# Kernel tuning notes

Measured on AMD Instinct MI355X. Metric: run time of the kernel, lower is better.

The kernel has to match this reference:

```python
import jax, jax.numpy as jnp
import numpy as np

N = 100000   # total nodes
E = 1600000  # edges
F_IN = 128   # num_features
HL1 = 128    # hidden
G = 100      # num graphs
GF = 16      # num_global_feats
GH = 32      # global_hl1 (hardcoded in module)


def _gcn_conv(x, W, b, src, dst, n):
    # PyG GCNConv: add self-loops, symmetric deg^{-1/2} normalization,
    # linear transform then normalized scatter-add aggregation, plus bias.
    h = x @ W  # [n, out]
    ones = jnp.ones(src.shape[0], x.dtype)
    deg = jax.ops.segment_sum(ones, dst, num_segments=n) + 1.0  # +1 for self-loop
    dinv = jnp.where(deg > 0, 1.0 / jnp.sqrt(deg), 0.0)
    norm = dinv[src] * dinv[dst]                      # [E]
    agg = jax.ops.segment_sum(h[src] * norm[:, None], dst, num_segments=n)
    agg = agg + h * (dinv * dinv)[:, None]            # self-loop messages (i->i)
    return agg + b


def setup_inputs() -> dict:
    key = jax.random.key(0)
    ks = jax.random.split(key, 24)
    inp = {}
    inp["x"] = jax.random.normal(ks[0], (N, F_IN), jnp.float32)
    inp["edge_index"] = jax.random.randint(ks[1], (2, E), 0, N, jnp.int64)
    inp["batch"] = jnp.sort(jax.random.randint(ks[2], (N,), 0, G, jnp.int32))
    inp["global_feats"] = jax.random.normal(ks[3], (G * GF,), jnp.float32)
    inp["num_graphs"] = G
    s = 0.05
    inp["conv1_W"] = jax.random.normal(ks[4], (F_IN, HL1), jnp.float32) * s
    inp["conv1_b"] = jnp.zeros((HL1,), jnp.float32)
    inp["conv2_W"] = jax.random.normal(ks[5], (HL1, HL1), jnp.float32) * s
    inp["conv2_b"] = jnp.zeros((HL1,), jnp.float32)
    inp["conv3_W"] = jax.random.normal(ks[6], (HL1, HL1), jnp.float32) * s
    inp["conv3_b"] = jnp.zeros((HL1,), jnp.float32)
    inp["conv4_W"] = jax.random.normal(ks[7], (HL1, HL1), jnp.float32) * s
    inp["conv4_b"] = jnp.zeros((HL1,), jnp.float32)
    inp["global1_W"] = jax.random.normal(ks[8], (GF, GH), jnp.float32) * s
    inp["global1_b"] = jnp.zeros((GH,), jnp.float32)
    inp["lin1_W"] = jax.random.normal(ks[9], (HL1, HL1), jnp.float32) * s
    inp["lin1_b"] = jnp.zeros((HL1,), jnp.float32)
    inp["lin2_W"] = jax.random.normal(ks[10], (HL1 + GH, HL1), jnp.float32) * s
    inp["lin2_b"] = jnp.zeros((HL1,), jnp.float32)
    inp["lin3_W"] = jax.random.normal(ks[11], (HL1, HL1), jnp.float32) * s
    inp["lin3_b"] = jnp.zeros((HL1,), jnp.float32)
    inp["lin4_W"] = jax.random.normal(ks[12], (HL1, 1), jnp.float32) * s
    inp["lin4_b"] = jnp.zeros((1,), jnp.float32)
    return inp


def reference(x, edge_index, batch, global_feats, num_graphs,
              conv1_W, conv1_b, conv2_W, conv2_b, conv3_W, conv3_b,
              conv4_W, conv4_b, global1_W, global1_b,
              lin1_W, lin1_b, lin2_W, lin2_b, lin3_W, lin3_b, lin4_W, lin4_b):
    src, dst = edge_index[0], edge_index[1]
    n = x.shape[0]
    relu = jax.nn.relu
    h = relu(_gcn_conv(x, conv1_W, conv1_b, src, dst, n))
    h = relu(_gcn_conv(h, conv2_W, conv2_b, src, dst, n))
    h = relu(_gcn_conv(h, conv3_W, conv3_b, src, dst, n))
    h = relu(_gcn_conv(h, conv4_W, conv4_b, src, dst, n))
    # per-graph sum pooling (vectorized segment-sum instead of python loop)
    pooled = jax.ops.segment_sum(h, batch, num_segments=num_graphs)  # [G, HL1]
    gfs = global_feats.reshape(num_graphs, -1)                        # [G, GF]
    g = relu(gfs @ global1_W + global1_b)                             # [G, GH]
    y = relu(pooled @ lin1_W + lin1_b)
    y = jnp.concatenate([y, g], axis=1)
    y = relu(y @ lin2_W + lin2_b)
    y = relu(y @ lin3_W + lin3_b)
    y = y @ lin4_W + lin4_b
    return y.squeeze(1)  # final_act == 'none'
```

## Files before the change

### kernel.cpp

```cpp
#include <hip/hip_runtime.h>
#include <hip/hip_bf16.h>

#define NN 100000
#define NE 1600000
#define FD 128
#define NG 100
#define GFD 16
#define GHD 32

#define NB 391
#define BCAP 5120

typedef __attribute__((ext_vector_type(8))) _Float16 f16x8;
typedef __attribute__((ext_vector_type(2))) _Float16 f16x2;
typedef __attribute__((ext_vector_type(4))) float f32x4;

static inline int cdiv(int a, int b) { return (a + b - 1) / b; }


__global__ void k_zero_int(int* __restrict__ p, int n) {
  int i = blockIdx.x * blockDim.x + threadIdx.x;
  if (i < n) p[i] = 0;
}

__global__ void k_zero_row(_Float16* __restrict__ Hs) {
  int t = threadIdx.x;
  if (t < FD) Hs[(size_t)NN * FD + t] = (_Float16)0.f;
}

__global__ __launch_bounds__(256) void k_binA(const int* __restrict__ src,
                                              const int* __restrict__ dst,
                                              int* __restrict__ gcur,
                                              unsigned int* __restrict__ stag) {
  __shared__ int cnt[NB];
  __shared__ int gbase[NB];
  __shared__ int cursor[NB];
  int t = threadIdx.x;
  for (int i = t; i < NB; i += 256) cnt[i] = 0;
  __syncthreads();
  int e0 = blockIdx.x * 2048;
  int s[8], d[8], b[8];
#pragma unroll
  for (int j = 0; j < 8; j++) {
    int e = e0 + j * 256 + t;
    if (e < NE) {
      s[j] = src[e];
      d[j] = dst[e];
      b[j] = d[j] >> 8;
      atomicAdd(&cnt[b[j]], 1);
    } else {
      b[j] = -1;
    }
  }
  __syncthreads();
  for (int i = t; i < NB; i += 256) {
    int c = cnt[i];
    gbase[i] = (c > 0) ? atomicAdd(&gcur[i], c) : 0;
    cursor[i] = 0;
  }
  __syncthreads();
#pragma unroll
  for (int j = 0; j < 8; j++) {
    if (b[j] >= 0) {
      int r = atomicAdd(&cursor[b[j]], 1);
      stag[(size_t)b[j] * BCAP + gbase[b[j]] + r] =
          ((unsigned int)s[j] << 8) | (unsigned int)(d[j] & 255);
    }
  }
}

__global__ __launch_bounds__(256) void k_binB(const unsigned int* __restrict__ stag,
                                              const int* __restrict__ gcur,
                                              int* __restrict__ deg,
                                              float* __restrict__ dinv) {
  __shared__ int h[256];
  int b = blockIdx.x;
  int t = threadIdx.x;
  h[t] = 0;
  __syncthreads();
  int n = gcur[b];
  const unsigned int* p = stag + (size_t)b * BCAP;
  for (int i = t; i < n; i += 256) atomicAdd(&h[p[i] & 255], 1);
  __syncthreads();
  int node = b * 256 + t;
  if (node < NN) {
    int dg = h[t];
    deg[node] = dg;
    dinv[node] = 1.0f / sqrtf((float)(dg + 1));
  }
}

__global__ __launch_bounds__(256) void k_scan1(const int* __restrict__ deg,
                                               int* __restrict__ offs,
                                               int* __restrict__ bsum) {
  __shared__ int sh[256];
  int b = blockIdx.x;
  int t = threadIdx.x;
  int base = b * 1024 + t * 4;
  int v0 = (base + 0 < NN) ? ((deg[base + 0] + 7) & ~7) : 0;
  int v1 = (base + 1 < NN) ? ((deg[base + 1] + 7) & ~7) : 0;
  int v2 = (base + 2 < NN) ? ((deg[base + 2] + 7) & ~7) : 0;
  int v3 = (base + 3 < NN) ? ((deg[base + 3] + 7) & ~7) : 0;
  int s = v0 + v1 + v2 + v3;
  sh[t] = s;
  __syncthreads();
  for (int off = 1; off < 256; off <<= 1) {
    int tv = (t >= off) ? sh[t - off] : 0;
    __syncthreads();
    sh[t] += tv;
    __syncthreads();
  }
  int excl = sh[t] - s;
  if (base + 0 < NN) offs[base + 0] = excl;
  if (base + 1 < NN) offs[base + 1] = excl + v0;
  if (base + 2 < NN) offs[base + 2] = excl + v0 + v1;
  if (base + 3 < NN) offs[base + 3] = excl + v0 + v1 + v2;
  if (t == 255) bsum[b] = sh[255];
}

__global__ __launch_bounds__(128) void k_scan2(int* __restrict__ bsum, int nb,
                                               int* __restrict__ ptot) {
  __shared__ int sh[128];
  int t = threadIdx.x;
  int v = (t < nb) ? bsum[t] : 0;
  sh[t] = v;
  __syncthreads();
  for (int off = 1; off < 128; off <<= 1) {
    int tv = (t >= off) ? sh[t - off] : 0;
    __syncthreads();
    sh[t] += tv;
    __syncthreads();
  }
  if (t < nb) bsum[t] = sh[t] - v;
  if (t == nb - 1) ptot[0] = sh[t];
}

__global__ void k_scan3(int* __restrict__ offs, const int* __restrict__ bsum,
                        const int* __restrict__ ptot) {
  int i = blockIdx.x * blockDim.x + threadIdx.x;
  if (i < NN) offs[i] = offs[i] + bsum[i >> 10];
  if (i == 0) offs[NN] = ptot[0];
}

__global__ __launch_bounds__(256) void k_binC(const unsigned int* __restrict__ stag,
                                              const int* __restrict__ gcur,
                                              const int* __restrict__ offs,
                                              int* __restrict__ ssrc) {
  __shared__ int cur[256];
  int b = blockIdx.x;
  int t = threadIdx.x;
  int node = b * 256 + t;
  cur[t] = (node < NN) ? offs[node] : 0;
  __syncthreads();
  int n = gcur[b];
  const unsigned int* p = stag + (size_t)b * BCAP;
  for (int i = t; i < n; i += 256) {
    unsigned int v = p[i];
    int pos = atomicAdd(&cur[v & 255], 1);
    ssrc[pos] = (int)(v >> 8);
  }
  __syncthreads();
  if (node < NN) {
    int end = offs[node + 1];
    for (int pos = cur[t]; pos < end; pos++) ssrc[pos] = NN;
  }
}


__global__ void k_cvt_w4(const float* __restrict__ W0, const float* __restrict__ W1,
                         const float* __restrict__ W2, const float* __restrict__ W3,
                         _Float16* __restrict__ Wf ) {
  int tt = blockIdx.x * blockDim.x + threadIdx.x;
  int layer = tt >> 14;
  int t = tt & 16383;
  const float* W = (layer == 0) ? W0 : (layer == 1) ? W1 : (layer == 2) ? W2 : W3;
  int i = t & 7;
  int l = (t >> 3) & 63;
  int nt = (t >> 9) & 7;
  int kb = (t >> 12) & 3;
  int k = kb * 32 + (l >> 4) * 8 + i;
  int n = nt * 16 + (l & 15);
  float w = W[k * FD + n];
  _Float16 hi = (_Float16)w;
  _Float16* dst = Wf + (size_t)layer * 32768;
  dst[t] = hi;
  dst[t + 16384] = (_Float16)(w - (float)hi);
}

__global__ __launch_bounds__(256) void k_gemm_mfma(
    const _Float16* __restrict__ Xh,
    const _Float16* __restrict__ Wfrag,
    const float* __restrict__ dinv,
    _Float16* __restrict__ Hs) {
  int tid = threadIdx.x;
  int lane = tid & 63;
  int wave = tid >> 6;
  int r0 = blockIdx.x * 64 + wave * 16;
  int arow = r0 + (lane & 15);
  int kgrp = lane >> 4;

  f32x4 acc[8];
#pragma unroll
  for (int nt = 0; nt < 8; nt++) acc[nt] = (f32x4){0.f, 0.f, 0.f, 0.f};

#pragma unroll
  for (int kb = 0; kb < 4; kb++) {
    f16x8 a;
    if (arow < NN) {
      a = *(const f16x8*)(Xh + (size_t)arow * FD + kb * 32 + kgrp * 8);
    } else {
      a = (f16x8){0, 0, 0, 0, 0, 0, 0, 0};
    }
    const _Float16* wp = Wfrag + ((size_t)(kb * 8) * 64 + lane) * 8;
#pragma unroll
    for (int nt = 0; nt < 8; nt++) {
      f16x8 bhi = *(const f16x8*)(wp + (size_t)nt * 64 * 8);
      f16x8 blo = *(const f16x8*)(wp + (size_t)nt * 64 * 8 + 16384);
      acc[nt] = __builtin_amdgcn_mfma_f32_16x16x32_f16(a, bhi, acc[nt], 0, 0, 0);
      acc[nt] = __builtin_amdgcn_mfma_f32_16x16x32_f16(a, blo, acc[nt], 0, 0, 0);
    }
  }

  int ccol = lane & 15;
  int rbase = r0 + (lane >> 4) * 4;
  float dv[4];
#pragma unroll
  for (int j = 0; j < 4; j++) dv[j] = (rbase + j < NN) ? dinv[rbase + j] : 0.f;
#pragma unroll
  for (int nt = 0; nt < 8; nt++) {
#pragma unroll
    for (int j = 0; j < 4; j++) {
      int r = rbase + j;
      if (r < NN) {
        Hs[(size_t)r * FD + nt * 16 + ccol] = (_Float16)(acc[nt][j] * dv[j]);
      }
    }
  }
}

__global__ __launch_bounds__(256) void k_gemm_mfma_f32(
    const float* __restrict__ X,
    const _Float16* __restrict__ Wfrag,
    const float* __restrict__ dinv,
    _Float16* __restrict__ Hs) {
  int tid = threadIdx.x;
  int lane = tid & 63;
  int wave = tid >> 6;
  int r0 = blockIdx.x * 64 + wave * 16;
  int arow = r0 + (lane & 15);
  int kgrp = lane >> 4;

  f32x4 acc[8];
#pragma unroll
  for (int nt = 0; nt < 8; nt++) acc[nt] = (f32x4){0.f, 0.f, 0.f, 0.f};

#pragma unroll
  for (int kb = 0; kb < 4; kb++) {
    f16x8 a;
    if (arow < NN) {
      const float4* xp = (const float4*)(X + (size_t)arow * FD + kb * 32 + kgrp * 8);
      float4 x0 = xp[0], x1 = xp[1];
      a = (f16x8){(_Float16)x0.x, (_Float16)x0.y, (_Float16)x0.z, (_Float16)x0.w,
                  (_Float16)x1.x, (_Float16)x1.y, (_Float16)x1.z, (_Float16)x1.w};
    } else {
      a = (f16x8){0, 0, 0, 0, 0, 0, 0, 0};
    }
    const _Float16* wp = Wfrag + ((size_t)(kb * 8) * 64 + lane) * 8;
#pragma unroll
    for (int nt = 0; nt < 8; nt++) {
      f16x8 bhi = *(const f16x8*)(wp + (size_t)nt * 64 * 8);
      f16x8 blo = *(const f16x8*)(wp + (size_t)nt * 64 * 8 + 16384);
      acc[nt] = __builtin_amdgcn_mfma_f32_16x16x32_f16(a, bhi, acc[nt], 0, 0, 0);
      acc[nt] = __builtin_amdgcn_mfma_f32_16x16x32_f16(a, blo, acc[nt], 0, 0, 0);
    }
  }

  int ccol = lane & 15;
  int rbase = r0 + (lane >> 4) * 4;
  float dv[4];
#pragma unroll
  for (int j = 0; j < 4; j++) dv[j] = (rbase + j < NN) ? dinv[rbase + j] : 0.f;
#pragma unroll
  for (int nt = 0; nt < 8; nt++) {
#pragma unroll
    for (int j = 0; j < 4; j++) {
      int r = rbase + j;
      if (r < NN) {
        Hs[(size_t)r * FD + nt * 16 + ccol] = (_Float16)(acc[nt][j] * dv[j]);
      }
    }
  }
}

__global__ __launch_bounds__(256) void k_agg(const _Float16* __restrict__ Hs,
                                             const float* __restrict__ dinv,
                                             const int* __restrict__ offs,
                                             const int* __restrict__ ssrc,
                                             const float* __restrict__ bias,
                                             _Float16* __restrict__ Bout) {
  int wave = threadIdx.x >> 6;
  int lane = threadIdx.x & 63;
  int node = blockIdx.x * 4 + wave;
  int g = lane >> 4;
  int c = lane & 15;

  int e0 = offs[node], e1 = offs[node + 1];
  int cnt = e1 - e0;
  int myidx = (lane < cnt) ? ssrc[e0 + lane] : NN;

  float acc[8];
#pragma unroll
  for (int k = 0; k < 8; k++) acc[k] = 0.f;

  for (int base = 0; base < cnt; base += 16) {
    int p = base + g * 4;
    int i0, i1, i2, i3;
    if (base < 64) {
      i0 = __builtin_amdgcn_ds_bpermute((p + 0) * 4, myidx);
      i1 = __builtin_amdgcn_ds_bpermute((p + 1) * 4, myidx);
      i2 = __builtin_amdgcn_ds_bpermute((p + 2) * 4, myidx);
      i3 = __builtin_amdgcn_ds_bpermute((p + 3) * 4, myidx);
    } else {
      i0 = (p + 0 < cnt) ? ssrc[e0 + p + 0] : NN;
      i1 = (p + 1 < cnt) ? ssrc[e0 + p + 1] : NN;
      i2 = (p + 2 < cnt) ? ssrc[e0 + p + 2] : NN;
      i3 = (p + 3 < cnt) ? ssrc[e0 + p + 3] : NN;
    }
    f16x8 v0 = *(const f16x8*)(Hs + (size_t)i0 * FD + c * 8);
    f16x8 v1 = *(const f16x8*)(Hs + (size_t)i1 * FD + c * 8);
    f16x8 v2 = *(const f16x8*)(Hs + (size_t)i2 * FD + c * 8);
    f16x8 v3 = *(const f16x8*)(Hs + (size_t)i3 * FD + c * 8);
#pragma unroll
    for (int k = 0; k < 8; k++) {
      acc[k] += ((float)v0[k] + (float)v1[k]) + ((float)v2[k] + (float)v3[k]);
    }
  }

#pragma unroll
  for (int k = 0; k < 8; k++) {
    acc[k] += __shfl_xor(acc[k], 16, 64);
    acc[k] += __shfl_xor(acc[k], 32, 64);
  }

  if (g == 0) {
    float di = dinv[node];
    f16x8 sf = *(const f16x8*)(Hs + (size_t)node * FD + c * 8);
    float4 b0 = *(const float4*)(bias + c * 8);
    float4 b1 = *(const float4*)(bias + c * 8 + 4);
    float bb[8] = {b0.x, b0.y, b0.z, b0.w, b1.x, b1.y, b1.z, b1.w};
    f16x8 o;
#pragma unroll
    for (int k = 0; k < 8; k++) {
      o[k] = (_Float16)fmaxf(fmaf(acc[k] + (float)sf[k], di, bb[k]), 0.f);
    }
    *(f16x8*)(Bout + (size_t)node * FD + c * 8) = o;
  }
}

__global__ __launch_bounds__(128) void k_pool(const _Float16* __restrict__ H,
                                              const int* __restrict__ batch,
                                              float* __restrict__ part) {
  int g = blockIdx.x >> 3;
  int s = blockIdx.x & 7;
  int start, end;
  {
    int lo = 0, hi = NN;
    while (lo < hi) { int m = (lo + hi) >> 1; if (batch[m] < g) lo = m + 1; else hi = m; }
    start = lo;
    lo = start; hi = NN;
    while (lo < hi) { int m = (lo + hi) >> 1; if (batch[m] < g + 1) lo = m + 1; else hi = m; }
    end = lo;
  }
  int cnt = end - start;
  int chunk = (cnt + 7) >> 3;
  int a = start + s * chunk;
  int bnd = a + chunk;
  if (bnd > end) bnd = end;
  int f = threadIdx.x;
  float acc = 0.f;
  for (int i = a; i < bnd; i++) acc += (float)H[(size_t)i * FD + f];
  part[(size_t)blockIdx.x * FD + f] = acc;
}

__global__ __launch_bounds__(128) void k_tail(
    const float* __restrict__ part, const float* __restrict__ gfeats,
    const float* __restrict__ W1, const float* __restrict__ b1,
    const float* __restrict__ Wg, const float* __restrict__ bg,
    const float* __restrict__ W2, const float* __restrict__ b2,
    const float* __restrict__ W3, const float* __restrict__ b3,
    const float* __restrict__ W4, const float* __restrict__ b4,
    float* __restrict__ out) {
  __shared__ float row[FD];
  __shared__ float y1[FD];
  __shared__ float gv[GHD];
  __shared__ float y2[FD];
  __shared__ float red[FD];
  int g = blockIdx.x, j = threadIdx.x;

  float p = 0.f;
  for (int s = 0; s < 8; s++) p += part[(size_t)(g * 8 + s) * FD + j];
  row[j] = p;
  if (j < GHD) {
    float a = bg[j];
    for (int k = 0; k < GFD; k++) a = fmaf(gfeats[g * GFD + k], Wg[k * GHD + j], a);
    gv[j] = fmaxf(a, 0.f);
  }
  __syncthreads();

  float a1 = b1[j];
  for (int k = 0; k < FD; k++) a1 = fmaf(row[k], W1[k * FD + j], a1);
  y1[j] = fmaxf(a1, 0.f);
  __syncthreads();

  float a2 = b2[j];
  for (int k = 0; k < FD; k++) a2 = fmaf(y1[k], W2[k * FD + j], a2);
  for (int k = 0; k < GHD; k++) a2 = fmaf(gv[k], W2[(FD + k) * FD + j], a2);
  y2[j] = fmaxf(a2, 0.f);
  __syncthreads();

  float a3 = b3[j];
  for (int k = 0; k < FD; k++) a3 = fmaf(y2[k], W3[k * FD + j], a3);
  float y3 = fmaxf(a3, 0.f);

  red[j] = y3 * W4[j];
  __syncthreads();
  for (int st = 64; st > 0; st >>= 1) {
    if (j < st) red[j] += red[j + st];
    __syncthreads();
  }
  if (j == 0) out[g] = red[0] + b4[0];
}

extern "C" void kernel_launch(void* const* d_in, const int* in_sizes, int n_in,
                              void* d_out, int out_size, void* d_ws, size_t ws_size,
                              hipStream_t stream) {
  const float* x      = (const float*)d_in[0];
  const int*   ei     = (const int*)d_in[1];
  const int*   batch  = (const int*)d_in[2];
  const float* gfeats = (const float*)d_in[3];
  const float* c1W = (const float*)d_in[5];  const float* c1b = (const float*)d_in[6];
  const float* c2W = (const float*)d_in[7];  const float* c2b = (const float*)d_in[8];
  const float* c3W = (const float*)d_in[9];  const float* c3b = (const float*)d_in[10];
  const float* c4W = (const float*)d_in[11]; const float* c4b = (const float*)d_in[12];
  const float* gW  = (const float*)d_in[13]; const float* gb  = (const float*)d_in[14];
  const float* l1W = (const float*)d_in[15]; const float* l1b = (const float*)d_in[16];
  const float* l2W = (const float*)d_in[17]; const float* l2b = (const float*)d_in[18];
  const float* l3W = (const float*)d_in[19]; const float* l3b = (const float*)d_in[20];
  const float* l4W = (const float*)d_in[21]; const float* l4b = (const float*)d_in[22];
  const int* srcp = ei;
  const int* dstp = ei + NE;
  float* out = (float*)d_out;

  char* p = (char*)d_ws;
  auto alloc = [&](size_t bytes) {
    char* r = p;
    p += (bytes + 255) & ~(size_t)255;
    return (void*)r;
  };
  _Float16* Hs  = (_Float16*)alloc((size_t)(NN + 1) * FD * 2);
  _Float16* Bb  = (_Float16*)alloc((size_t)NN * FD * 2);
  _Float16* Wf  = (_Float16*)alloc((size_t)4 * 32768 * 2);
  float* dinv = (float*)alloc((size_t)NN * 4);
  int*   deg  = (int*)alloc((size_t)NN * 4);
  int*   offs = (int*)alloc((size_t)(NN + 1) * 4);
  int*   ssrc = (int*)alloc((size_t)(NE + 8 * NN) * 4);
  int*   bsum = (int*)alloc(128 * 4);
  int*   ptot = (int*)alloc(256);
  float* part = (float*)alloc((size_t)NG * 8 * FD * 4);
  unsigned int* stag = (unsigned int*)alloc((size_t)NB * BCAP * 4);
  int*   gcur = (int*)alloc((size_t)NB * 4);

  int nb_scan = cdiv(NN, 1024);

  k_zero_int<<<cdiv(NB, 256), 256, 0, stream>>>(gcur, NB);
  k_zero_row<<<1, 128, 0, stream>>>(Hs);
  k_binA<<<cdiv(NE, 2048), 256, 0, stream>>>(srcp, dstp, gcur, stag);
  k_binB<<<NB, 256, 0, stream>>>(stag, gcur, deg, dinv);
  k_scan1<<<nb_scan, 256, 0, stream>>>(deg, offs, bsum);
  k_scan2<<<1, 128, 0, stream>>>(bsum, nb_scan, ptot);
  k_scan3<<<cdiv(NN, 256), 256, 0, stream>>>(offs, bsum, ptot);
  k_binC<<<NB, 256, 0, stream>>>(stag, gcur, offs, ssrc);

  k_cvt_w4<<<256, 256, 0, stream>>>(c1W, c2W, c3W, c4W, Wf);

  int gemm_grid = cdiv(NN, 64);
  const float* bs4[4] = {c1b, c2b, c3b, c4b};
  k_gemm_mfma_f32<<<gemm_grid, 256, 0, stream>>>(x, Wf, dinv, Hs);
  k_agg<<<NN / 4, 256, 0, stream>>>(Hs, dinv, offs, ssrc, bs4[0], Bb);
  for (int l = 1; l < 4; l++) {
    k_gemm_mfma<<<gemm_grid, 256, 0, stream>>>(Bb, Wf + (size_t)l * 32768, dinv, Hs);
    k_agg<<<NN / 4, 256, 0, stream>>>(Hs, dinv, offs, ssrc, bs4[l], Bb);
  }

  k_pool<<<NG * 8, 128, 0, stream>>>(Bb, batch, part);
  k_tail<<<NG, 128, 0, stream>>>(part, gfeats, l1W, l1b, gW, gb, l2W, l2b,
                                 l3W, l3b, l4W, l4b, out);
}
```

Measured before the change: 492.6 us.

## Slice feature matrices into 16-column planes to localize aggregation gathers

The hidden and output feature buffers move from row-major [N,128] to eight column-slab planes of [N,16] each. The aggregation kernel now gives each block a single slab, with 16 edges per wave step each reading 32 bytes. The intent is for each slab's working set (about 3.2 MB) to stay resident in cache while the random neighbor gathers run. The cost is that every edge index list is re-read eight times, and the GEMM, pooling and zero-row code all had to adopt the slab addressing.

Measured after the change: 941.1 us. 1.91x slower.

```diff
diff --git a/kernel.cpp b/kernel.cpp
--- a/kernel.cpp
+++ b/kernel.cpp
@@ -11,8 +11,11 @@
 #define NB 391
 #define BCAP 5120
 
+#define SSTRIDE ((size_t)(NN + 1) * 16)
+#define BSTRIDE ((size_t)NN * 16)
+
 typedef __attribute__((ext_vector_type(8))) _Float16 f16x8;
-typedef __attribute__((ext_vector_type(2))) _Float16 f16x2;
+typedef __attribute__((ext_vector_type(4))) _Float16 f16x4;
 typedef __attribute__((ext_vector_type(4))) float f32x4;
 
 static inline int cdiv(int a, int b) { return (a + b - 1) / b; }
@@ -25,7 +28,8 @@
 
 __global__ void k_zero_row(_Float16* __restrict__ Hs) {
   int t = threadIdx.x;
-  if (t < FD) Hs[(size_t)NN * FD + t] = (_Float16)0.f;
+  int q = t >> 4, c = t & 15;
+  Hs[(size_t)q * SSTRIDE + (size_t)NN * 16 + c] = (_Float16)0.f;
 }
 
 __global__ __launch_bounds__(256) void k_binA(const int* __restrict__ src,
@@ -188,7 +192,7 @@
 }
 
 __global__ __launch_bounds__(256) void k_gemm_mfma(
-    const _Float16* __restrict__ Xh,
+    const _Float16* __restrict__ Xs,
     const _Float16* __restrict__ Wfrag,
     const float* __restrict__ dinv,
     _Float16* __restrict__ Hs) {
@@ -207,7 +211,8 @@
   for (int kb = 0; kb < 4; kb++) {
     f16x8 a;
     if (arow < NN) {
-      a = *(const f16x8*)(Xh + (size_t)arow * FD + kb * 32 + kgrp * 8);
+      int q = kb * 2 + (kgrp >> 1);
+      a = *(const f16x8*)(Xs + (size_t)q * BSTRIDE + (size_t)arow * 16 + (kgrp & 1) * 8);
     } else {
       a = (f16x8){0, 0, 0, 0, 0, 0, 0, 0};
     }
@@ -232,7 +237,7 @@
     for (int j = 0; j < 4; j++) {
       int r = rbase + j;
       if (r < NN) {
-        Hs[(size_t)r * FD + nt * 16 + ccol] = (_Float16)(acc[nt][j] * dv[j]);
+        Hs[(size_t)nt * SSTRIDE + (size_t)r * 16 + ccol] = (_Float16)(acc[nt][j] * dv[j]);
       }
     }
   }
@@ -286,74 +291,65 @@
     for (int j = 0; j < 4; j++) {
       int r = rbase + j;
       if (r < NN) {
-        Hs[(size_t)r * FD + nt * 16 + ccol] = (_Float16)(acc[nt][j] * dv[j]);
+        Hs[(size_t)nt * SSTRIDE + (size_t)r * 16 + ccol] = (_Float16)(acc[nt][j] * dv[j]);
       }
     }
   }
 }
 
-__global__ __launch_bounds__(256) void k_agg(const _Float16* __restrict__ Hs,
-                                             const float* __restrict__ dinv,
-                                             const int* __restrict__ offs,
-                                             const int* __restrict__ ssrc,
-                                             const float* __restrict__ bias,
-                                             _Float16* __restrict__ Bout) {
+__global__ __launch_bounds__(256) void k_agg_s(const _Float16* __restrict__ Hs,
+                                               const float* __restrict__ dinv,
+                                               const int* __restrict__ offs,
+                                               const int* __restrict__ ssrc,
+                                               const float* __restrict__ bias,
+                                               _Float16* __restrict__ Bout) {
+  int q = blockIdx.x & 7;
+  int chunk = blockIdx.x >> 3;
   int wave = threadIdx.x >> 6;
   int lane = threadIdx.x & 63;
-  int node = blockIdx.x * 4 + wave;
-  int g = lane >> 4;
-  int c = lane & 15;
-
-  int e0 = offs[node], e1 = offs[node + 1];
-  int cnt = e1 - e0;
-  int myidx = (lane < cnt) ? ssrc[e0 + lane] : NN;
-
-  float acc[8];
-#pragma unroll
-  for (int k = 0; k < 8; k++) acc[k] = 0.f;
-
-  for (int base = 0; base < cnt; base += 16) {
-    int p = base + g * 4;
-    int i0, i1, i2, i3;
-    if (base < 64) {
-      i0 = __builtin_amdgcn_ds_bpermute((p + 0) * 4, myidx);
-      i1 = __builtin_amdgcn_ds_bpermute((p + 1) * 4, myidx);
-      i2 = __builtin_amdgcn_ds_bpermute((p + 2) * 4, myidx);
-      i3 = __builtin_amdgcn_ds_bpermute((p + 3) * 4, myidx);
-    } else {
-      i0 = (p + 0 < cnt) ? ssrc[e0 + p + 0] : NN;
-      i1 = (p + 1 < cnt) ? ssrc[e0 + p + 1] : NN;
-      i2 = (p + 2 < cnt) ? ssrc[e0 + p + 2] : NN;
-      i3 = (p + 3 < cnt) ? ssrc[e0 + p + 3] : NN;
-    }
-    f16x8 v0 = *(const f16x8*)(Hs + (size_t)i0 * FD + c * 8);
-    f16x8 v1 = *(const f16x8*)(Hs + (size_t)i1 * FD + c * 8);
-    f16x8 v2 = *(const f16x8*)(Hs + (size_t)i2 * FD + c * 8);
-    f16x8 v3 = *(const f16x8*)(Hs + (size_t)i3 * FD + c * 8);
-#pragma unroll
-    for (int k = 0; k < 8; k++) {
-      acc[k] += ((float)v0[k] + (float)v1[k]) + ((float)v2[k] + (float)v3[k]);
-    }
-  }
-
-#pragma unroll
-  for (int k = 0; k < 8; k++) {
-    acc[k] += __shfl_xor(acc[k], 16, 64);
-    acc[k] += __shfl_xor(acc[k], 32, 64);
-  }
-
-  if (g == 0) {
-    float di = dinv[node];
-    f16x8 sf = *(const f16x8*)(Hs + (size_t)node * FD + c * 8);
-    float4 b0 = *(const float4*)(bias + c * 8);
-    float4 b1 = *(const float4*)(bias + c * 8 + 4);
-    float bb[8] = {b0.x, b0.y, b0.z, b0.w, b1.x, b1.y, b1.z, b1.w};
-    f16x8 o;
-#pragma unroll
-    for (int k = 0; k < 8; k++) {
-      o[k] = (_Float16)fmaxf(fmaf(acc[k] + (float)sf[k], di, bb[k]), 0.f);
-    }
-    *(f16x8*)(Bout + (size_t)node * FD + c * 8) = o;
+  int sub = lane >> 2;
+  int cl = lane & 3;
+  const _Float16* hsq = Hs + (size_t)q * SSTRIDE;
+  _Float16* boq = Bout + (size_t)q * BSTRIDE;
+  float4 bb = *(const float4*)(bias + q * 16 + cl * 4);
+  int node0 = chunk * 32 + wave * 8;
+
+  for (int n = 0; n < 8; n++) {
+    int node = node0 + n;
+    int e0 = offs[node], e1 = offs[node + 1];
+    int cnt = e1 - e0;
+    int myidx = (lane < cnt) ? ssrc[e0 + lane] : NN;
+    float a0 = 0.f, a1 = 0.f, a2 = 0.f, a3 = 0.f;
+    for (int base = 0; base < cnt; base += 16) {
+      int sidx;
+      if (base < 64) {
+        sidx = __builtin_amdgcn_ds_bpermute((base + sub) << 2, myidx);
+      } else {
+        sidx = (base + sub < cnt) ? ssrc[e0 + base + sub] : NN;
+      }
+      f16x4 v = *(const f16x4*)(hsq + (size_t)sidx * 16 + cl * 4);
+      a0 += (float)v[0];
+      a1 += (float)v[1];
+      a2 += (float)v[2];
+      a3 += (float)v[3];
+    }
+#pragma unroll
+    for (int m = 4; m <= 32; m <<= 1) {
+      a0 += __shfl_xor(a0, m, 64);
+      a1 += __shfl_xor(a1, m, 64);
+      a2 += __shfl_xor(a2, m, 64);
+      a3 += __shfl_xor(a3, m, 64);
+    }
+    if (sub == 0) {
+      float di = dinv[node];
+      f16x4 sf = *(const f16x4*)(hsq + (size_t)node * 16 + cl * 4);
+      f16x4 o;
+      o[0] = (_Float16)fmaxf(fmaf(a0 + (float)sf[0], di, bb.x), 0.f);
+      o[1] = (_Float16)fmaxf(fmaf(a1 + (float)sf[1], di, bb.y), 0.f);
+      o[2] = (_Float16)fmaxf(fmaf(a2 + (float)sf[2], di, bb.z), 0.f);
+      o[3] = (_Float16)fmaxf(fmaf(a3 + (float)sf[3], di, bb.w), 0.f);
+      *(f16x4*)(boq + (size_t)node * 16 + cl * 4) = o;
+    }
   }
 }
 
@@ -377,8 +373,9 @@
   int bnd = a + chunk;
   if (bnd > end) bnd = end;
   int f = threadIdx.x;
+  const _Float16* hq = H + (size_t)(f >> 4) * BSTRIDE + (f & 15);
   float acc = 0.f;
-  for (int i = a; i < bnd; i++) acc += (float)H[(size_t)i * FD + f];
+  for (int i = a; i < bnd; i++) acc += (float)hq[(size_t)i * 16];
   part[(size_t)blockIdx.x * FD + f] = acc;
 }
 
@@ -457,8 +454,8 @@
     p += (bytes + 255) & ~(size_t)255;
     return (void*)r;
   };
-  _Float16* Hs  = (_Float16*)alloc((size_t)(NN + 1) * FD * 2);
-  _Float16* Bb  = (_Float16*)alloc((size_t)NN * FD * 2);
+  _Float16* Hs  = (_Float16*)alloc((size_t)8 * SSTRIDE * 2);
+  _Float16* Bb  = (_Float16*)alloc((size_t)8 * BSTRIDE * 2);
   _Float16* Wf  = (_Float16*)alloc((size_t)4 * 32768 * 2);
   float* dinv = (float*)alloc((size_t)NN * 4);
   int*   deg  = (int*)alloc((size_t)NN * 4);
@@ -484,12 +481,13 @@
   k_cvt_w4<<<256, 256, 0, stream>>>(c1W, c2W, c3W, c4W, Wf);
 
   int gemm_grid = cdiv(NN, 64);
+  int agg_grid = 8 * (NN / 32);
   const float* bs4[4] = {c1b, c2b, c3b, c4b};
   k_gemm_mfma_f32<<<gemm_grid, 256, 0, stream>>>(x, Wf, dinv, Hs);
-  k_agg<<<NN / 4, 256, 0, stream>>>(Hs, dinv, offs, ssrc, bs4[0], Bb);
+  k_agg_s<<<agg_grid, 256, 0, stream>>>(Hs, dinv, offs, ssrc, bs4[0], Bb);
   for (int l = 1; l < 4; l++) {
     k_gemm_mfma<<<gemm_grid, 256, 0, stream>>>(Bb, Wf + (size_t)l * 32768, dinv, Hs);
-    k_agg<<<NN / 4, 256, 0, stream>>>(Hs, dinv, offs, ssrc, bs4[l], Bb);
+    k_agg_s<<<agg_grid, 256, 0, stream>>>(Hs, dinv, offs, ssrc, bs4[l], Bb);
   }
 
   k_pool<<<NG * 8, 128, 0, stream>>>(Bb, batch, part);
```

## Fuse GCN aggregation with next layer's GEMM via LDS tile, merge small kernels

Applied to the files above, without the earlier changes.

Aggregation for a 64-node tile is computed into an LDS buffer and immediately multiplied by the next layer's weights with MFMA, so the intermediate activation no longer goes to global memory and back. This uses ping-pong Hs buffers. The scan-fixup kernel is folded into binC and the two init kernels are merged, cutting launch count. The trade-off is that each wave now aggregates 16 nodes serially before the GEMM phase, which may reduce latency hiding for the gather compared with the old one-node-per-wave aggregation kernel.

New measurement: 511.8 us. 1.04x slower.

```diff
diff --git a/kernel.cpp b/kernel.cpp
--- a/kernel.cpp
+++ b/kernel.cpp
@@ -11,21 +11,21 @@
 #define NB 391
 #define BCAP 5120
 
+#define LROW 136
+
 typedef __attribute__((ext_vector_type(8))) _Float16 f16x8;
-typedef __attribute__((ext_vector_type(2))) _Float16 f16x2;
 typedef __attribute__((ext_vector_type(4))) float f32x4;
 
 static inline int cdiv(int a, int b) { return (a + b - 1) / b; }
 
-
-__global__ void k_zero_int(int* __restrict__ p, int n) {
-  int i = blockIdx.x * blockDim.x + threadIdx.x;
-  if (i < n) p[i] = 0;
-}
-
-__global__ void k_zero_row(_Float16* __restrict__ Hs) {
+__global__ void k_init(int* __restrict__ gcur, _Float16* __restrict__ HsA,
+                       _Float16* __restrict__ HsB) {
   int t = threadIdx.x;
-  if (t < FD) Hs[(size_t)NN * FD + t] = (_Float16)0.f;
+  if (t < NB) gcur[t] = 0;
+  if (t < FD) {
+    HsA[(size_t)NN * FD + t] = (_Float16)0.f;
+    HsB[(size_t)NN * FD + t] = (_Float16)0.f;
+  }
 }
 
 __global__ __launch_bounds__(256) void k_binA(const int* __restrict__ src,
@@ -135,22 +135,25 @@
   if (t == nb - 1) ptot[0] = sh[t];
 }
 
-__global__ void k_scan3(int* __restrict__ offs, const int* __restrict__ bsum,
-                        const int* __restrict__ ptot) {
-  int i = blockIdx.x * blockDim.x + threadIdx.x;
-  if (i < NN) offs[i] = offs[i] + bsum[i >> 10];
-  if (i == 0) offs[NN] = ptot[0];
-}
-
 __global__ __launch_bounds__(256) void k_binC(const unsigned int* __restrict__ stag,
                                               const int* __restrict__ gcur,
-                                              const int* __restrict__ offs,
+                                              const int* __restrict__ offsp,
+                                              const int* __restrict__ bsum,
+                                              const int* __restrict__ ptot,
+                                              int* __restrict__ offs,
                                               int* __restrict__ ssrc) {
   __shared__ int cur[256];
+  __shared__ int nxt[256];
   int b = blockIdx.x;
   int t = threadIdx.x;
   int node = b * 256 + t;
-  cur[t] = (node < NN) ? offs[node] : 0;
+  int of = 0, ofn = 0;
+  if (node < NN) {
+    of = offsp[node] + bsum[node >> 10];
+    ofn = (node + 1 < NN) ? (offsp[node + 1] + bsum[(node + 1) >> 10]) : ptot[0];
+  }
+  cur[t] = of;
+  nxt[t] = ofn;
   __syncthreads();
   int n = gcur[b];
   const unsigned int* p = stag + (size_t)b * BCAP;
@@ -161,11 +164,11 @@
   }
   __syncthreads();
   if (node < NN) {
-    int end = offs[node + 1];
-    for (int pos = cur[t]; pos < end; pos++) ssrc[pos] = NN;
-  }
-}
-
+    offs[node] = of;
+    if (node == NN - 1) offs[NN] = ptot[0];
+    for (int pos = cur[t]; pos < nxt[t]; pos++) ssrc[pos] = NN;
+  }
+}
 
 __global__ void k_cvt_w4(const float* __restrict__ W0, const float* __restrict__ W1,
                          const float* __restrict__ W2, const float* __restrict__ W3,
@@ -187,57 +190,6 @@
   dst[t + 16384] = (_Float16)(w - (float)hi);
 }
 
-__global__ __launch_bounds__(256) void k_gemm_mfma(
-    const _Float16* __restrict__ Xh,
-    const _Float16* __restrict__ Wfrag,
-    const float* __restrict__ dinv,
-    _Float16* __restrict__ Hs) {
-  int tid = threadIdx.x;
-  int lane = tid & 63;
-  int wave = tid >> 6;
-  int r0 = blockIdx.x * 64 + wave * 16;
-  int arow = r0 + (lane & 15);
-  int kgrp = lane >> 4;
-
-  f32x4 acc[8];
-#pragma unroll
-  for (int nt = 0; nt < 8; nt++) acc[nt] = (f32x4){0.f, 0.f, 0.f, 0.f};
-
-#pragma unroll
-  for (int kb = 0; kb < 4; kb++) {
-    f16x8 a;
-    if (arow < NN) {
-      a = *(const f16x8*)(Xh + (size_t)arow * FD + kb * 32 + kgrp * 8);
-    } else {
-      a = (f16x8){0, 0, 0, 0, 0, 0, 0, 0};
-    }
-    const _Float16* wp = Wfrag + ((size_t)(kb * 8) * 64 + lane) * 8;
-#pragma unroll
-    for (int nt = 0; nt < 8; nt++) {
-      f16x8 bhi = *(const f16x8*)(wp + (size_t)nt * 64 * 8);
-      f16x8 blo = *(const f16x8*)(wp + (size_t)nt * 64 * 8 + 16384);
-      acc[nt] = __builtin_amdgcn_mfma_f32_16x16x32_f16(a, bhi, acc[nt], 0, 0, 0);
-      acc[nt] = __builtin_amdgcn_mfma_f32_16x16x32_f16(a, blo, acc[nt], 0, 0, 0);
-    }
-  }
-
-  int ccol = lane & 15;
-  int rbase = r0 + (lane >> 4) * 4;
-  float dv[4];
-#pragma unroll
-  for (int j = 0; j < 4; j++) dv[j] = (rbase + j < NN) ? dinv[rbase + j] : 0.f;
-#pragma unroll
-  for (int nt = 0; nt < 8; nt++) {
-#pragma unroll
-    for (int j = 0; j < 4; j++) {
-      int r = rbase + j;
-      if (r < NN) {
-        Hs[(size_t)r * FD + nt * 16 + ccol] = (_Float16)(acc[nt][j] * dv[j]);
-      }
-    }
-  }
-}
-
 __global__ __launch_bounds__(256) void k_gemm_mfma_f32(
     const float* __restrict__ X,
     const _Float16* __restrict__ Wfrag,
@@ -287,6 +239,121 @@
       int r = rbase + j;
       if (r < NN) {
         Hs[(size_t)r * FD + nt * 16 + ccol] = (_Float16)(acc[nt][j] * dv[j]);
+      }
+    }
+  }
+}
+
+__global__ __launch_bounds__(256) void k_fused(
+    const _Float16* __restrict__ HsIn,
+    const float* __restrict__ dinv,
+    const int* __restrict__ offs,
+    const int* __restrict__ ssrc,
+    const float* __restrict__ bias,
+    const _Float16* __restrict__ Wfrag,
+    _Float16* __restrict__ HsOut) {
+  __shared__ _Float16 LB[64][LROW];
+  int tid = threadIdx.x;
+  int lane = tid & 63;
+  int wave = tid >> 6;
+  int g = lane >> 4;
+  int c = lane & 15;
+
+  for (int i = 0; i < 16; i++) {
+    int node = blockIdx.x * 64 + wave * 16 + i;
+    int lrow = wave * 16 + i;
+    if (node < NN) {
+      int e0 = offs[node], e1 = offs[node + 1];
+      int cnt = e1 - e0;
+      int myidx = (lane < cnt) ? ssrc[e0 + lane] : NN;
+      float acc[8];
+#pragma unroll
+      for (int k = 0; k < 8; k++) acc[k] = 0.f;
+      for (int base = 0; base < cnt; base += 16) {
+        int p = base + g * 4;
+        int i0, i1, i2, i3;
+        if (base < 64) {
+          i0 = __builtin_amdgcn_ds_bpermute((p + 0) * 4, myidx);
+          i1 = __builtin_amdgcn_ds_bpermute((p + 1) * 4, myidx);
+          i2 = __builtin_amdgcn_ds_bpermute((p + 2) * 4, myidx);
+          i3 = __builtin_amdgcn_ds_bpermute((p + 3) * 4, myidx);
+        } else {
+          i0 = (p + 0 < cnt) ? ssrc[e0 + p + 0] : NN;
+          i1 = (p + 1 < cnt) ? ssrc[e0 + p + 1] : NN;
+          i2 = (p + 2 < cnt) ? ssrc[e0 + p + 2] : NN;
+          i3 = (p + 3 < cnt) ? ssrc[e0 + p + 3] : NN;
+        }
+        f16x8 v0 = *(const f16x8*)(HsIn + (size_t)i0 * FD + c * 8);
+        f16x8 v1 = *(const f16x8*)(HsIn + (size_t)i1 * FD + c * 8);
+        f16x8 v2 = *(const f16x8*)(HsIn + (size_t)i2 * FD + c * 8);
+        f16x8 v3 = *(const f16x8*)(HsIn + (size_t)i3 * FD + c * 8);
+#pragma unroll
+        for (int k = 0; k < 8; k++) {
+          acc[k] += ((float)v0[k] + (float)v1[k]) + ((float)v2[k] + (float)v3[k]);
+        }
+      }
+#pragma unroll
+      for (int k = 0; k < 8; k++) {
+        acc[k] += __shfl_xor(acc[k], 16, 64);
+        acc[k] += __shfl_xor(acc[k], 32, 64);
+      }
+      if (g == 0) {
+        float di = dinv[node];
+        f16x8 sf = *(const f16x8*)(HsIn + (size_t)node * FD + c * 8);
+        float4 b0 = *(const float4*)(bias + c * 8);
+        float4 b1 = *(const float4*)(bias + c * 8 + 4);
+        float bb[8] = {b0.x, b0.y, b0.z, b0.w, b1.x, b1.y, b1.z, b1.w};
+        f16x8 o;
+#pragma unroll
+        for (int k = 0; k < 8; k++) {
+          o[k] = (_Float16)fmaxf(fmaf(acc[k] + (float)sf[k], di, bb[k]), 0.f);
+        }
+        *(f16x8*)(&LB[lrow][c * 8]) = o;
+      }
+    } else {
+      if (g == 0) {
+        f16x8 z = (f16x8){0, 0, 0, 0, 0, 0, 0, 0};
+        *(f16x8*)(&LB[lrow][c * 8]) = z;
+      }
+    }
+  }
+  __syncthreads();
+
+  int kgrp = lane >> 4;
+  int arl = wave * 16 + (lane & 15);
+  int ccol = lane & 15;
+  int rbl = wave * 16 + (lane >> 4) * 4;
+  int rglob = blockIdx.x * 64 + rbl;
+  float dv[4];
+#pragma unroll
+  for (int j = 0; j < 4; j++) dv[j] = (rglob + j < NN) ? dinv[rglob + j] : 0.f;
+
+#pragma unroll
+  for (int half = 0; half < 2; half++) {
+    f32x4 acc[4];
+#pragma unroll
+    for (int nt = 0; nt < 4; nt++) acc[nt] = (f32x4){0.f, 0.f, 0.f, 0.f};
+#pragma unroll
+    for (int kb = 0; kb < 4; kb++) {
+      f16x8 a = *(const f16x8*)(&LB[arl][kb * 32 + kgrp * 8]);
+#pragma unroll
+      for (int nt = 0; nt < 4; nt++) {
+        const _Float16* wp = Wfrag + ((size_t)(kb * 8 + half * 4 + nt) * 64 + lane) * 8;
+        f16x8 bhi = *(const f16x8*)(wp);
+        f16x8 blo = *(const f16x8*)(wp + 16384);
+        acc[nt] = __builtin_amdgcn_mfma_f32_16x16x32_f16(a, bhi, acc[nt], 0, 0, 0);
+        acc[nt] = __builtin_amdgcn_mfma_f32_16x16x32_f16(a, blo, acc[nt], 0, 0, 0);
+      }
+    }
+#pragma unroll
+    for (int nt = 0; nt < 4; nt++) {
+#pragma unroll
+      for (int j = 0; j < 4; j++) {
+        int r = rglob + j;
+        if (r < NN) {
+          HsOut[(size_t)r * FD + (half * 4 + nt) * 16 + ccol] =
+              (_Float16)(acc[nt][j] * dv[j]);
+        }
       }
     }
   }
@@ -457,13 +524,14 @@
     p += (bytes + 255) & ~(size_t)255;
     return (void*)r;
   };
-  _Float16* Hs  = (_Float16*)alloc((size_t)(NN + 1) * FD * 2);
+  _Float16* HsA = (_Float16*)alloc((size_t)(NN + 1) * FD * 2);
+  _Float16* HsB = (_Float16*)alloc((size_t)(NN + 1) * FD * 2);
   _Float16* Bb  = (_Float16*)alloc((size_t)NN * FD * 2);
   _Float16* Wf  = (_Float16*)alloc((size_t)4 * 32768 * 2);
   float* dinv = (float*)alloc((size_t)NN * 4);
   int*   deg  = (int*)alloc((size_t)NN * 4);
   int*   offs = (int*)alloc((size_t)(NN + 1) * 4);
-  int*   ssrc = (int*)alloc((size_t)(NE + 8 * NN) * 4);
+  int*   ssrc = (int*)alloc((size_t)(NE + 8 * NN + 64) * 4);
   int*   bsum = (int*)alloc(128 * 4);
   int*   ptot = (int*)alloc(256);
   float* part = (float*)alloc((size_t)NG * 8 * FD * 4);
@@ -472,25 +540,24 @@
 
   int nb_scan = cdiv(NN, 1024);
 
-  k_zero_int<<<cdiv(NB, 256), 256, 0, stream>>>(gcur, NB);
-  k_zero_row<<<1, 128, 0, stream>>>(Hs);
+  k_init<<<1, 512, 0, stream>>>(gcur, HsA, HsB);
   k_binA<<<cdiv(NE, 2048), 256, 0, stream>>>(srcp, dstp, gcur, stag);
   k_binB<<<NB, 256, 0, stream>>>(stag, gcur, deg, dinv);
   k_scan1<<<nb_scan, 256, 0, stream>>>(deg, offs, bsum);
   k_scan2<<<1, 128, 0, stream>>>(bsum, nb_scan, ptot);
-  k_scan3<<<cdiv(NN, 256), 256, 0, stream>>>(offs, bsum, ptot);
-  k_binC<<<NB, 256, 0, stream>>>(stag, gcur, offs, ssrc);
+  k_binC<<<NB, 256, 0, stream>>>(stag, gcur, offs, bsum, ptot, offs, ssrc);
 
   k_cvt_w4<<<256, 256, 0, stream>>>(c1W, c2W, c3W, c4W, Wf);
 
-  int gemm_grid = cdiv(NN, 64);
-  const float* bs4[4] = {c1b, c2b, c3b, c4b};
-  k_gemm_mfma_f32<<<gemm_grid, 256, 0, stream>>>(x, Wf, dinv, Hs);
-  k_agg<<<NN / 4, 256, 0, stream>>>(Hs, dinv, offs, ssrc, bs4[0], Bb);
-  for (int l = 1; l < 4; l++) {
-    k_gemm_mfma<<<gemm_grid, 256, 0, stream>>>(Bb, Wf + (size_t)l * 32768, dinv, Hs);
-    k_agg<<<NN / 4, 256, 0, stream>>>(Hs, dinv, offs, ssrc, bs4[l], Bb);
-  }
+  int grid64 = cdiv(NN, 64);
+  k_gemm_mfma_f32<<<grid64, 256, 0, stream>>>(x, Wf, dinv, HsA);
+  k_fused<<<grid64, 256, 0, stream>>>(HsA, dinv, offs, ssrc, c1b,
+                                      Wf + (size_t)1 * 32768, HsB);
+  k_fused<<<grid64, 256, 0, stream>>>(HsB, dinv, offs, ssrc, c2b,
+                                      Wf + (size_t)2 * 32768, HsA);
+  k_fused<<<grid64, 256, 0, stream>>>(HsA, dinv, offs, ssrc, c3b,
+                                      Wf + (size_t)3 * 32768, HsB);
+  k_agg<<<NN / 4, 256, 0, stream>>>(HsB, dinv, offs, ssrc, c4b, Bb);
 
   k_pool<<<NG * 8, 128, 0, stream>>>(Bb, batch, part);
   k_tail<<<NG, 128, 0, stream>>>(part, gfeats, l1W, l1b, gW, gb, l2W, l2b,
```

## Fuse degree, scan and CSR offset passes into fewer preprocessing kernels

Applied to the files above, without the earlier changes.

Merges the two zeroing kernels into one init launch. Folds the per-block exclusive scan into the degree-histogram kernel, and moves the final offset add into the CSR fill kernel. This removes the deg array, the scan1 and scan3 kernels and their global memory round trips. The goal is lower launch count and less preprocessing traffic, at the cost of a 512-wide second-level scan and a slightly more complex binC.

Result: no change. 487.0 us (-1.1%).

```diff
diff --git a/kernel.cpp b/kernel.cpp
--- a/kernel.cpp
+++ b/kernel.cpp
@@ -12,19 +12,13 @@
 #define BCAP 5120
 
 typedef __attribute__((ext_vector_type(8))) _Float16 f16x8;
-typedef __attribute__((ext_vector_type(2))) _Float16 f16x2;
 typedef __attribute__((ext_vector_type(4))) float f32x4;
 
 static inline int cdiv(int a, int b) { return (a + b - 1) / b; }
 
-
-__global__ void k_zero_int(int* __restrict__ p, int n) {
-  int i = blockIdx.x * blockDim.x + threadIdx.x;
-  if (i < n) p[i] = 0;
-}
-
-__global__ void k_zero_row(_Float16* __restrict__ Hs) {
+__global__ void k_init(int* __restrict__ gcur, _Float16* __restrict__ Hs) {
   int t = threadIdx.x;
+  if (t < NB) gcur[t] = 0;
   if (t < FD) Hs[(size_t)NN * FD + t] = (_Float16)0.f;
 }
 
@@ -71,9 +65,11 @@
 
 __global__ __launch_bounds__(256) void k_binB(const unsigned int* __restrict__ stag,
                                               const int* __restrict__ gcur,
-                                              int* __restrict__ deg,
-                                              float* __restrict__ dinv) {
+                                              float* __restrict__ dinv,
+                                              int* __restrict__ offsp,
+                                              int* __restrict__ bsum) {
   __shared__ int h[256];
+  __shared__ int sh[256];
   int b = blockIdx.x;
   int t = threadIdx.x;
   h[t] = 0;
@@ -83,26 +79,10 @@
   for (int i = t; i < n; i += 256) atomicAdd(&h[p[i] & 255], 1);
   __syncthreads();
   int node = b * 256 + t;
-  if (node < NN) {
-    int dg = h[t];
-    deg[node] = dg;
-    dinv[node] = 1.0f / sqrtf((float)(dg + 1));
-  }
-}
-
-__global__ __launch_bounds__(256) void k_scan1(const int* __restrict__ deg,
-                                               int* __restrict__ offs,
-                                               int* __restrict__ bsum) {
-  __shared__ int sh[256];
-  int b = blockIdx.x;
-  int t = threadIdx.x;
-  int base = b * 1024 + t * 4;
-  int v0 = (base + 0 < NN) ? ((deg[base + 0] + 7) & ~7) : 0;
-  int v1 = (base + 1 < NN) ? ((deg[base + 1] + 7) & ~7) : 0;
-  int v2 = (base + 2 < NN) ? ((deg[base + 2] + 7) & ~7) : 0;
-  int v3 = (base + 3 < NN) ? ((deg[base + 3] + 7) & ~7) : 0;
-  int s = v0 + v1 + v2 + v3;
-  sh[t] = s;
+  int dg = h[t];
+  int pd = (node < NN) ? ((dg + 7) & ~7) : 0;
+  if (node < NN) dinv[node] = 1.0f / sqrtf((float)(dg + 1));
+  sh[t] = pd;
   __syncthreads();
   for (int off = 1; off < 256; off <<= 1) {
     int tv = (t >= off) ? sh[t - off] : 0;
@@ -110,47 +90,46 @@
     sh[t] += tv;
     __syncthreads();
   }
-  int excl = sh[t] - s;
-  if (base + 0 < NN) offs[base + 0] = excl;
-  if (base + 1 < NN) offs[base + 1] = excl + v0;
-  if (base + 2 < NN) offs[base + 2] = excl + v0 + v1;
-  if (base + 3 < NN) offs[base + 3] = excl + v0 + v1 + v2;
+  if (node < NN) offsp[node] = sh[t] - pd;
   if (t == 255) bsum[b] = sh[255];
 }
 
-__global__ __launch_bounds__(128) void k_scan2(int* __restrict__ bsum, int nb,
+__global__ __launch_bounds__(512) void k_scan2(int* __restrict__ bsum,
                                                int* __restrict__ ptot) {
-  __shared__ int sh[128];
+  __shared__ int sh[512];
   int t = threadIdx.x;
-  int v = (t < nb) ? bsum[t] : 0;
+  int v = (t < NB) ? bsum[t] : 0;
   sh[t] = v;
   __syncthreads();
-  for (int off = 1; off < 128; off <<= 1) {
+  for (int off = 1; off < 512; off <<= 1) {
     int tv = (t >= off) ? sh[t - off] : 0;
     __syncthreads();
     sh[t] += tv;
     __syncthreads();
   }
-  if (t < nb) bsum[t] = sh[t] - v;
-  if (t == nb - 1) ptot[0] = sh[t];
-}
-
-__global__ void k_scan3(int* __restrict__ offs, const int* __restrict__ bsum,
-                        const int* __restrict__ ptot) {
-  int i = blockIdx.x * blockDim.x + threadIdx.x;
-  if (i < NN) offs[i] = offs[i] + bsum[i >> 10];
-  if (i == 0) offs[NN] = ptot[0];
+  if (t < NB) bsum[t] = sh[t] - v;
+  if (t == NB - 1) ptot[0] = sh[t];
 }
 
 __global__ __launch_bounds__(256) void k_binC(const unsigned int* __restrict__ stag,
                                               const int* __restrict__ gcur,
-                                              const int* __restrict__ offs,
+                                              const int* __restrict__ offsp,
+                                              const int* __restrict__ bsum,
+                                              const int* __restrict__ ptot,
+                                              int* __restrict__ offs,
                                               int* __restrict__ ssrc) {
   __shared__ int cur[256];
+  __shared__ int nxt[256];
   int b = blockIdx.x;
   int t = threadIdx.x;
   int node = b * 256 + t;
-  cur[t] = (node < NN) ? offs[node] : 0;
+  int of = 0, ofn = 0;
+  if (node < NN) {
+    of = offsp[node] + bsum[node >> 8];
+    ofn = (node + 1 < NN) ? (offsp[node + 1] + bsum[(node + 1) >> 8]) : ptot[0];
+  }
+  cur[t] = of;
+  nxt[t] = ofn;
   __syncthreads();
   int n = gcur[b];
   const unsigned int* p = stag + (size_t)b * BCAP;
@@ -161,11 +140,11 @@
   }
   __syncthreads();
   if (node < NN) {
-    int end = offs[node + 1];
-    for (int pos = cur[t]; pos < end; pos++) ssrc[pos] = NN;
-  }
-}
-
+    offs[node] = of;
+    if (node == NN - 1) offs[NN] = ptot[0];
+    for (int pos = cur[t]; pos < nxt[t]; pos++) ssrc[pos] = NN;
+  }
+}
 
 __global__ void k_cvt_w4(const float* __restrict__ W0, const float* __restrict__ W1,
                          const float* __restrict__ W2, const float* __restrict__ W3,
@@ -461,25 +440,20 @@
   _Float16* Bb  = (_Float16*)alloc((size_t)NN * FD * 2);
   _Float16* Wf  = (_Float16*)alloc((size_t)4 * 32768 * 2);
   float* dinv = (float*)alloc((size_t)NN * 4);
-  int*   deg  = (int*)alloc((size_t)NN * 4);
+  int*   offsp = (int*)alloc((size_t)NN * 4);
   int*   offs = (int*)alloc((size_t)(NN + 1) * 4);
-  int*   ssrc = (int*)alloc((size_t)(NE + 8 * NN) * 4);
-  int*   bsum = (int*)alloc(128 * 4);
+  int*   ssrc = (int*)alloc((size_t)(NE + 8 * NN + 64) * 4);
+  int*   bsum = (int*)alloc(512 * 4);
   int*   ptot = (int*)alloc(256);
   float* part = (float*)alloc((size_t)NG * 8 * FD * 4);
   unsigned int* stag = (unsigned int*)alloc((size_t)NB * BCAP * 4);
   int*   gcur = (int*)alloc((size_t)NB * 4);
 
-  int nb_scan = cdiv(NN, 1024);
-
-  k_zero_int<<<cdiv(NB, 256), 256, 0, stream>>>(gcur, NB);
-  k_zero_row<<<1, 128, 0, stream>>>(Hs);
+  k_init<<<1, 512, 0, stream>>>(gcur, Hs);
   k_binA<<<cdiv(NE, 2048), 256, 0, stream>>>(srcp, dstp, gcur, stag);
-  k_binB<<<NB, 256, 0, stream>>>(stag, gcur, deg, dinv);
-  k_scan1<<<nb_scan, 256, 0, stream>>>(deg, offs, bsum);
-  k_scan2<<<1, 128, 0, stream>>>(bsum, nb_scan, ptot);
-  k_scan3<<<cdiv(NN, 256), 256, 0, stream>>>(offs, bsum, ptot);
-  k_binC<<<NB, 256, 0, stream>>>(stag, gcur, offs, ssrc);
+  k_binB<<<NB, 256, 0, stream>>>(stag, gcur, dinv, offsp, bsum);
+  k_scan2<<<1, 512, 0, stream>>>(bsum, ptot);
+  k_binC<<<NB, 256, 0, stream>>>(stag, gcur, offsp, bsum, ptot, offs, ssrc);
 
   k_cvt_w4<<<256, 256, 0, stream>>>(c1W, c2W, c3W, c4W, Wf);
 
```
